# Kernel tuning notes

Measured on AMD Instinct MI355X. Metric: run time of the kernel, lower is better.

Reference implementation:

```python
import jax, jax.numpy as jnp
import numpy as np

N_CB, VOCAB, CDIM = 8, 1024, 16
DECAY = 0.99
EPS = 1e-5


def setup_inputs() -> dict:
    key = jax.random.key(0)
    k1, k2, k3 = jax.random.split(key, 3)
    z = jax.random.normal(k1, (8, N_CB * CDIM, 32, 32), jnp.float32)
    codebooks = jax.random.normal(k2, (N_CB, VOCAB, CDIM), jnp.float32) * 0.02
    ema_count = jnp.zeros((N_CB, VOCAB), jnp.float32)
    ema_weight = jax.random.normal(k3, (N_CB, VOCAB, CDIM), jnp.float32) * 0.02
    return {"z": z, "codebooks": codebooks, "ema_count": ema_count, "ema_weight": ema_weight}


def reference(z, codebooks, ema_count, ema_weight):
    B, D, H, W = z.shape
    # (b d h w) -> (b h w, n_cb, cdim): matches rearrange + chunk(dim=-1)
    zp = z.transpose(0, 2, 3, 1).reshape(B * H * W, N_CB, CDIM)
    # squared distances (N, C, V): |z|^2 - 2 z.cb + |cb|^2
    d2 = (jnp.sum(zp * zp, axis=-1, keepdims=True)
          - 2.0 * jnp.einsum('ncd,cvd->ncv', zp, codebooks)
          + jnp.sum(codebooks * codebooks, axis=-1)[None, :, :])
    idx = jnp.argmin(d2, axis=-1)                      # (N, C) int
    zq = codebooks[jnp.arange(N_CB)[None, :], idx]     # (N, C, d) gather

    # --- EMA codebook update (training-mode math, no grad) ---
    idx_c = idx.T                                      # (C, N)
    zp_c = zp.transpose(1, 0, 2)                       # (C, N, d)
    counts = jax.vmap(lambda i: jnp.zeros((VOCAB,), jnp.float32).at[i].add(1.0))(idx_c)
    sums = jax.vmap(lambda i, x: jnp.zeros((VOCAB, CDIM), jnp.float32).at[i].add(x))(idx_c, zp_c)
    new_count = DECAY * ema_count + (1.0 - DECAY) * counts
    new_weight = DECAY * ema_weight + (1.0 - DECAY) * sums
    n = jnp.sum(new_count, axis=-1, keepdims=True)     # (C, 1)
    count = (new_count + EPS) / (n + VOCAB * EPS) * n  # Laplace-smoothed counts
    new_codebooks = new_weight / count[..., None]

    # commitment: mean over codebooks of per-part MSE == global MSE (equal part sizes)
    commitment = jnp.mean((zp - jax.lax.stop_gradient(zq)) ** 2)

    # straight-through estimator
    zq_st = zp + jax.lax.stop_gradient(zq - zp)        # (N, C, d)
    quantized = zq_st.reshape(B, H, W, D).transpose(0, 3, 1, 2)
    indices = idx.reshape(B, H, W, N_CB).transpose(0, 3, 1, 2)  # (B, C, H, W)
    return quantized, indices, commitment, new_codebooks, new_count, new_weight
```

## Files before the change

kernel.cpp:

```cpp
#include <hip/hip_runtime.h>


#define NCB   8
#define VOCAB 1024
#define CDIM  16
#define NPIX  8192
#define HW    1024

#define OFF_QUANT  0
#define OFF_IDX    1048576
#define OFF_COMMIT 1114112
#define OFF_NCB    1114113
#define OFF_NCNT   1245185
#define OFF_NWT    1253377

#define WS_CNTP_OFF 0
#define WS_SUMP_OFF (NCB * 2 * VOCAB)
#define WS_CARR_OFF (NCB * 2 * VOCAB + NCB * CDIM * 2 * VOCAB)

__device__ __forceinline__ float npsum16(const float m[16]) {
#pragma clang fp contract(off)
  float r0 = m[0] + m[8];
  float r1 = m[1] + m[9];
  float r2 = m[2] + m[10];
  float r3 = m[3] + m[11];
  float r4 = m[4] + m[12];
  float r5 = m[5] + m[13];
  float r6 = m[6] + m[14];
  float r7 = m[7] + m[15];
  return ((r0 + r1) + (r2 + r3)) + ((r4 + r5) + (r6 + r7));
}

__device__ __forceinline__ float npsum16sq(const float a[16]) {
#pragma clang fp contract(off)
  float m[16];
#pragma unroll
  for (int d = 0; d < 16; ++d) m[d] = a[d] * a[d];
  return npsum16(m);
}

__device__ __forceinline__ void proc_entry(const float zv[16],
                                           const float e[16], float c2v,
                                           float z2, int idx, float& best,
                                           int& bi) {
#pragma clang fp contract(off)
  float m[16];
#pragma unroll
  for (int d = 0; d < 16; ++d) m[d] = zv[d] * e[d];
  float l0 = (m[0] + m[4]) + (m[8] + m[12]);
  float l1 = (m[1] + m[5]) + (m[9] + m[13]);
  float l2 = (m[2] + m[6]) + (m[10] + m[14]);
  float l3 = (m[3] + m[7]) + (m[11] + m[15]);
  const float dot = (l0 + l1) + (l2 + l3);
  const float d2 = (z2 - 2.0f * dot) + c2v;
  const bool lt = d2 < best;
  best = lt ? d2 : best;
  bi = lt ? idx : bi;
}

__global__ __launch_bounds__(512, 4) void k_assign(
    const float* __restrict__ z, const float* __restrict__ cb,
    float* __restrict__ out, float* __restrict__ ws_commit_arr) {
  __shared__ float s_c2[VOCAB];
  __shared__ float s_best[8 * 128];
  __shared__ int s_bi[8 * 128];
  __shared__ float s_red[2];

  const int c = blockIdx.x >> 6;
  const int pchunk = blockIdx.x & 63;
  const int t = threadIdx.x;
  const int pix = t & 63;
  const int w = t >> 6;
  const int wu = __builtin_amdgcn_readfirstlane(w);

  const float* cbc = cb + (size_t)c * VOCAB * CDIM;

  for (int v = t; v < VOCAB; v += 512) {
    float e[16];
#pragma unroll
    for (int d = 0; d < 16; ++d) e[d] = cbc[(size_t)v * CDIM + d];
    s_c2[v] = npsum16sq(e);
  }

  const int nbase = pchunk * 128;
  const int b = nbase >> 10;
  const int hwb = nbase & 1023;

  const float* zbase = z + ((size_t)(b * 128 + c * 16)) * HW + hwb + pix;
  float zv[2][16];
  float z2[2];
#pragma unroll
  for (int r = 0; r < 2; ++r) {
#pragma unroll
    for (int d = 0; d < 16; ++d) zv[r][d] = zbase[(size_t)d * HW + r * 64];
    z2[r] = npsum16sq(zv[r]);
  }

  __syncthreads();

  const int vbase = wu * 128;
  const float* ep = cbc + (size_t)vbase * CDIM;

  float best[2] = {INFINITY, INFINITY};
  int bi[2] = {0, 0};

#pragma unroll 2
  for (int k = 0; k < 128; k += 2) {
    float ea[16], eb[16];
#pragma unroll
    for (int d = 0; d < 16; ++d) ea[d] = ep[(size_t)k * CDIM + d];
#pragma unroll
    for (int d = 0; d < 16; ++d) eb[d] = ep[(size_t)(k + 1) * CDIM + d];
    const float cv0 = s_c2[vbase + k];
    const float cv1 = s_c2[vbase + k + 1];
    proc_entry(zv[0], ea, cv0, z2[0], vbase + k, best[0], bi[0]);
    proc_entry(zv[1], ea, cv0, z2[1], vbase + k, best[1], bi[1]);
    proc_entry(zv[0], eb, cv1, z2[0], vbase + k + 1, best[0], bi[0]);
    proc_entry(zv[1], eb, cv1, z2[1], vbase + k + 1, best[1], bi[1]);
  }

#pragma unroll
  for (int r = 0; r < 2; ++r) {
    s_best[w * 128 + r * 64 + pix] = best[r];
    s_bi[w * 128 + r * 64 + pix] = bi[r];
  }
  __syncthreads();

  if (t < 128) {
    const int r = t >> 6;
    float bb = s_best[t];
    int bbi = s_bi[t];
#pragma unroll
    for (int s = 1; s < 8; ++s) {
      const float ob = s_best[s * 128 + t];
      const int oi = s_bi[s * 128 + t];
      const bool take = (ob < bb) || (ob == bb && oi < bbi);
      bb = take ? ob : bb;
      bbi = take ? oi : bbi;
    }

    const int hw = hwb + t;
    const float* qe = cbc + (size_t)bbi * CDIM;
    float comm = 0.f;
#pragma unroll
    for (int d = 0; d < 16; ++d) {
      float zq = qe[d];
      float diff, qst;
      {
#pragma clang fp contract(off)
        diff = zv[r][d] - zq;
        qst = zv[r][d] + (zq - zv[r][d]);
      }
      comm += diff * diff;
      out[OFF_QUANT + ((size_t)(b * 128 + c * 16 + d)) * HW + hw] = qst;
    }
    out[OFF_IDX + ((size_t)(b * NCB + c)) * HW + hw] = (float)bbi;

#pragma unroll
    for (int off = 32; off; off >>= 1) comm += __shfl_down(comm, off);
    if ((t & 63) == 0) s_red[t >> 6] = comm;
  }
  __syncthreads();
  if (t == 0) ws_commit_arr[blockIdx.x] = s_red[0] + s_red[1];
}

__global__ __launch_bounds__(1024, 4) void k_stats(
    const float* __restrict__ z, const float* __restrict__ outbuf,
    float* __restrict__ ws_counts_p, float* __restrict__ ws_sums_p) {
  __shared__ float s_sum[VOCAB];
  __shared__ float s_cnt[VOCAB];
  const int c = blockIdx.x >> 5;
  const int d = (blockIdx.x >> 1) & 15;
  const int half = blockIdx.x & 1;
  const int t = threadIdx.x;

  s_sum[t] = 0.f;
  if (d == 0) s_cnt[t] = 0.f;

  int bidx[4];
  float zval[4];
#pragma unroll
  for (int k = 0; k < 4; ++k) {
    const int bb = half * 4 + k;
    bidx[k] = (int)outbuf[OFF_IDX + ((size_t)(bb * NCB + c)) * HW + t];
    zval[k] = z[((size_t)(bb * 128 + c * 16 + d)) * HW + t];
  }
  __syncthreads();

#pragma unroll
  for (int k = 0; k < 4; ++k) {
    atomicAdd(&s_sum[bidx[k]], zval[k]);
    if (d == 0) atomicAdd(&s_cnt[bidx[k]], 1.0f);
  }
  __syncthreads();

  ws_sums_p[((size_t)((c * CDIM + d) * 2 + half)) * VOCAB + t] = s_sum[t];
  if (d == 0) ws_counts_p[(c * 2 + half) * VOCAB + t] = s_cnt[t];
}

__global__ __launch_bounds__(256) void k_update(
    const float* __restrict__ ema_count, const float* __restrict__ ema_weight,
    const float* __restrict__ ws_counts_p, const float* __restrict__ ws_sums_p,
    const float* __restrict__ ws_commit_arr, float* __restrict__ out) {
  const int c = blockIdx.x >> 3;
  const int part = blockIdx.x & 7;
  const int t = threadIdx.x;
  __shared__ float s_red[4];
  __shared__ float s_n;
  __shared__ double s_dred[4];

  const float* cp0 = ws_counts_p + (c * 2 + 0) * VOCAB;
  const float* cp1 = ws_counts_p + (c * 2 + 1) * VOCAB;

  float psum = 0.f;
#pragma unroll
  for (int k = 0; k < 4; ++k) {
    const int v = k * 256 + t;
    psum += 0.99f * ema_count[c * VOCAB + v] + 0.01f * (cp0[v] + cp1[v]);
  }
#pragma unroll
  for (int off = 32; off; off >>= 1) psum += __shfl_down(psum, off);
  if ((t & 63) == 0) s_red[t >> 6] = psum;
  __syncthreads();
  if (t == 0) s_n = (s_red[0] + s_red[1]) + (s_red[2] + s_red[3]);
  __syncthreads();
  const float nsum = s_n;
  const float veps = 0.01024f;

  if (t < 128) {
    const int v = part * 128 + t;
    out[OFF_NCNT + c * VOCAB + v] =
        0.99f * ema_count[c * VOCAB + v] + 0.01f * (cp0[v] + cp1[v]);
  }

#pragma unroll
  for (int k = 0; k < 8; ++k) {
    const int i = part * 2048 + k * 256 + t;
    const int v = i >> 4;
    const int d = i & 15;
    const float nc =
        0.99f * ema_count[c * VOCAB + v] + 0.01f * (cp0[v] + cp1[v]);
    const float cnt = (nc + 1e-5f) / (nsum + veps) * nsum;
    const size_t gi = (size_t)c * VOCAB * CDIM + i;
    const float s0 = ws_sums_p[((size_t)((c * CDIM + d) * 2 + 0)) * VOCAB + v];
    const float s1 = ws_sums_p[((size_t)((c * CDIM + d) * 2 + 1)) * VOCAB + v];
    const float nw = 0.99f * ema_weight[gi] + 0.01f * (s0 + s1);
    out[OFF_NWT + gi] = nw;
    out[OFF_NCB + gi] = nw / cnt;
  }

  if (blockIdx.x == 0) {
    double ps = 0.0;
#pragma unroll
    for (int k = 0; k < 2; ++k) ps += (double)ws_commit_arr[k * 256 + t];
#pragma unroll
    for (int off = 32; off; off >>= 1) ps += __shfl_down(ps, off);
    if ((t & 63) == 0) s_dred[t >> 6] = ps;
    __syncthreads();
    if (t == 0)
      out[OFF_COMMIT] =
          (float)(((s_dred[0] + s_dred[1]) + (s_dred[2] + s_dred[3])) /
                  1048576.0);
  }
}

extern "C" void kernel_launch(void* const* d_in, const int* in_sizes, int n_in,
                              void* d_out, int out_size, void* d_ws,
                              size_t ws_size, hipStream_t stream) {
  const float* z = (const float*)d_in[0];
  const float* codebooks = (const float*)d_in[1];
  const float* ema_count = (const float*)d_in[2];
  const float* ema_weight = (const float*)d_in[3];
  float* out = (float*)d_out;

  float* wsf = (float*)d_ws;
  float* ws_counts_p = wsf + WS_CNTP_OFF;
  float* ws_sums_p = wsf + WS_SUMP_OFF;
  float* ws_commit_arr = wsf + WS_CARR_OFF;


  k_assign<<<dim3(512), dim3(512), 0, stream>>>(z, codebooks, out,
                                                ws_commit_arr);
  k_stats<<<dim3(256), dim3(1024), 0, stream>>>(z, out, ws_counts_p,
                                                ws_sums_p);
  k_update<<<dim3(64), dim3(256), 0, stream>>>(ema_count, ema_weight,
                                               ws_counts_p, ws_sums_p,
                                               ws_commit_arr, out);
}
```

Measured before the change: 131.2 us.

## Fuse EMA stats histogram and codebook update into one kernel

Replaces the separate stats and update kernels with one fused kernel. Each of 128 blocks handles one (codebook, dim) pair, builds the full per-code count and sum histogram over all 8192 pixels in shared memory, then writes the EMA count, weight and normalized codebook directly. This removes one launch and the workspace round trip for the partial sums. In exchange there are half as many blocks, each doing twice as many shared-memory atomics, with the count histogram recomputed redundantly in all 16 dim blocks of a codebook, and stores to the weight output strided by 16.

```diff
diff --git a/kernel.cpp b/kernel.cpp
--- a/kernel.cpp
+++ b/kernel.cpp
@@ -14,9 +14,7 @@
 #define OFF_NCNT   1245185
 #define OFF_NWT    1253377
 
-#define WS_CNTP_OFF 0
-#define WS_SUMP_OFF (NCB * 2 * VOCAB)
-#define WS_CARR_OFF (NCB * 2 * VOCAB + NCB * CDIM * 2 * VOCAB)
+#define WS_CARR_OFF 0
 
 __device__ __forceinline__ float npsum16(const float m[16]) {
 #pragma clang fp contract(off)
@@ -164,103 +162,92 @@
   if (t == 0) ws_commit_arr[blockIdx.x] = s_red[0] + s_red[1];
 }
 
-__global__ __launch_bounds__(1024, 4) void k_stats(
+__global__ __launch_bounds__(512, 4) void k_fused(
     const float* __restrict__ z, const float* __restrict__ outbuf,
-    float* __restrict__ ws_counts_p, float* __restrict__ ws_sums_p) {
+    const float* __restrict__ ema_count, const float* __restrict__ ema_weight,
+    const float* __restrict__ ws_commit_arr, float* __restrict__ out) {
+  __shared__ float s_cnt[VOCAB];
   __shared__ float s_sum[VOCAB];
-  __shared__ float s_cnt[VOCAB];
-  const int c = blockIdx.x >> 5;
-  const int d = (blockIdx.x >> 1) & 15;
-  const int half = blockIdx.x & 1;
+  __shared__ float s_red[8];
+  __shared__ float s_n;
+  __shared__ double s_dred[8];
+
+  const int c = blockIdx.x >> 4;
+  const int d = blockIdx.x & 15;
   const int t = threadIdx.x;
-
+  const int lane = t & 63;
+  const int wv = t >> 6;
+
+  s_cnt[t] = 0.f;
+  s_cnt[512 + t] = 0.f;
   s_sum[t] = 0.f;
-  if (d == 0) s_cnt[t] = 0.f;
-
-  int bidx[4];
-  float zval[4];
-#pragma unroll
-  for (int k = 0; k < 4; ++k) {
-    const int bb = half * 4 + k;
-    bidx[k] = (int)outbuf[OFF_IDX + ((size_t)(bb * NCB + c)) * HW + t];
-    zval[k] = z[((size_t)(bb * 128 + c * 16 + d)) * HW + t];
-  }
-  __syncthreads();
-
-#pragma unroll
-  for (int k = 0; k < 4; ++k) {
-    atomicAdd(&s_sum[bidx[k]], zval[k]);
-    if (d == 0) atomicAdd(&s_cnt[bidx[k]], 1.0f);
-  }
-  __syncthreads();
-
-  ws_sums_p[((size_t)((c * CDIM + d) * 2 + half)) * VOCAB + t] = s_sum[t];
-  if (d == 0) ws_counts_p[(c * 2 + half) * VOCAB + t] = s_cnt[t];
-}
-
-__global__ __launch_bounds__(256) void k_update(
-    const float* __restrict__ ema_count, const float* __restrict__ ema_weight,
-    const float* __restrict__ ws_counts_p, const float* __restrict__ ws_sums_p,
-    const float* __restrict__ ws_commit_arr, float* __restrict__ out) {
-  const int c = blockIdx.x >> 3;
-  const int part = blockIdx.x & 7;
-  const int t = threadIdx.x;
-  __shared__ float s_red[4];
-  __shared__ float s_n;
-  __shared__ double s_dred[4];
-
-  const float* cp0 = ws_counts_p + (c * 2 + 0) * VOCAB;
-  const float* cp1 = ws_counts_p + (c * 2 + 1) * VOCAB;
-
-  float psum = 0.f;
-#pragma unroll
-  for (int k = 0; k < 4; ++k) {
-    const int v = k * 256 + t;
-    psum += 0.99f * ema_count[c * VOCAB + v] + 0.01f * (cp0[v] + cp1[v]);
-  }
+  s_sum[512 + t] = 0.f;
+  __syncthreads();
+
+#pragma unroll
+  for (int ph = 0; ph < 2; ++ph) {
+    int bidx[8];
+    float zval[8];
+#pragma unroll
+    for (int k = 0; k < 8; ++k) {
+      const int p = (ph * 8 + k) * 512 + t;
+      const int bb = p >> 10;
+      const int hw = p & 1023;
+      bidx[k] = (int)outbuf[OFF_IDX + ((size_t)(bb * NCB + c)) * HW + hw];
+      zval[k] = z[((size_t)(bb * 128 + c * 16 + d)) * HW + hw];
+    }
+#pragma unroll
+    for (int k = 0; k < 8; ++k) {
+      atomicAdd(&s_cnt[bidx[k]], 1.0f);
+      atomicAdd(&s_sum[bidx[k]], zval[k]);
+    }
+  }
+  __syncthreads();
+
+  const float nc0 = 0.99f * ema_count[c * VOCAB + t] + 0.01f * s_cnt[t];
+  const float nc1 =
+      0.99f * ema_count[c * VOCAB + 512 + t] + 0.01f * s_cnt[512 + t];
+  if (d == 0) {
+    out[OFF_NCNT + c * VOCAB + t] = nc0;
+    out[OFF_NCNT + c * VOCAB + 512 + t] = nc1;
+  }
+
+  float psum = nc0 + nc1;
 #pragma unroll
   for (int off = 32; off; off >>= 1) psum += __shfl_down(psum, off);
-  if ((t & 63) == 0) s_red[t >> 6] = psum;
-  __syncthreads();
-  if (t == 0) s_n = (s_red[0] + s_red[1]) + (s_red[2] + s_red[3]);
+  if (lane == 0) s_red[wv] = psum;
+  __syncthreads();
+  if (t == 0) {
+    float s = ((s_red[0] + s_red[1]) + (s_red[2] + s_red[3])) +
+              ((s_red[4] + s_red[5]) + (s_red[6] + s_red[7]));
+    s_n = s;
+  }
   __syncthreads();
   const float nsum = s_n;
   const float veps = 0.01024f;
 
-  if (t < 128) {
-    const int v = part * 128 + t;
-    out[OFF_NCNT + c * VOCAB + v] =
-        0.99f * ema_count[c * VOCAB + v] + 0.01f * (cp0[v] + cp1[v]);
-  }
-
-#pragma unroll
-  for (int k = 0; k < 8; ++k) {
-    const int i = part * 2048 + k * 256 + t;
-    const int v = i >> 4;
-    const int d = i & 15;
-    const float nc =
-        0.99f * ema_count[c * VOCAB + v] + 0.01f * (cp0[v] + cp1[v]);
+#pragma unroll
+  for (int j = 0; j < 2; ++j) {
+    const int v = j * 512 + t;
+    const float nc = j ? nc1 : nc0;
     const float cnt = (nc + 1e-5f) / (nsum + veps) * nsum;
-    const size_t gi = (size_t)c * VOCAB * CDIM + i;
-    const float s0 = ws_sums_p[((size_t)((c * CDIM + d) * 2 + 0)) * VOCAB + v];
-    const float s1 = ws_sums_p[((size_t)((c * CDIM + d) * 2 + 1)) * VOCAB + v];
-    const float nw = 0.99f * ema_weight[gi] + 0.01f * (s0 + s1);
+    const size_t gi = (size_t)c * VOCAB * CDIM + (size_t)v * CDIM + d;
+    const float nw = 0.99f * ema_weight[gi] + 0.01f * s_sum[v];
     out[OFF_NWT + gi] = nw;
     out[OFF_NCB + gi] = nw / cnt;
   }
 
   if (blockIdx.x == 0) {
-    double ps = 0.0;
-#pragma unroll
-    for (int k = 0; k < 2; ++k) ps += (double)ws_commit_arr[k * 256 + t];
+    double ps = (double)ws_commit_arr[t];
 #pragma unroll
     for (int off = 32; off; off >>= 1) ps += __shfl_down(ps, off);
-    if ((t & 63) == 0) s_dred[t >> 6] = ps;
+    if (lane == 0) s_dred[wv] = ps;
     __syncthreads();
-    if (t == 0)
-      out[OFF_COMMIT] =
-          (float)(((s_dred[0] + s_dred[1]) + (s_dred[2] + s_dred[3])) /
-                  1048576.0);
+    if (t == 0) {
+      double sd = ((s_dred[0] + s_dred[1]) + (s_dred[2] + s_dred[3])) +
+                  ((s_dred[4] + s_dred[5]) + (s_dred[6] + s_dred[7]));
+      out[OFF_COMMIT] = (float)(sd / 1048576.0);
+    }
   }
 }
 
@@ -273,17 +260,11 @@
   const float* ema_weight = (const float*)d_in[3];
   float* out = (float*)d_out;
 
-  float* wsf = (float*)d_ws;
-  float* ws_counts_p = wsf + WS_CNTP_OFF;
-  float* ws_sums_p = wsf + WS_SUMP_OFF;
-  float* ws_commit_arr = wsf + WS_CARR_OFF;
+  float* ws_commit_arr = (float*)d_ws + WS_CARR_OFF;
 
 
   k_assign<<<dim3(512), dim3(512), 0, stream>>>(z, codebooks, out,
                                                 ws_commit_arr);
-  k_stats<<<dim3(256), dim3(1024), 0, stream>>>(z, out, ws_counts_p,
-                                                ws_sums_p);
-  k_update<<<dim3(64), dim3(256), 0, stream>>>(ema_count, ema_weight,
-                                               ws_counts_p, ws_sums_p,
+  k_fused<<<dim3(128), dim3(512), 0, stream>>>(z, out, ema_count, ema_weight,
                                                ws_commit_arr, out);
 }
```

New measurement: 141.8 us. +8.1%, slower.
